# Kernel optimization log

Hardware: AMD Instinct MI355X
Metric: run time of the kernel (lower is better)

## Reference

```python
import jax, jax.numpy as jnp
import numpy as np

COMMITMENT_COST = 0.25
NUM_CODES = 4096
EMBED_DIM = 64


def setup_inputs() -> dict:
    key = jax.random.key(0)
    k1, k2 = jax.random.split(key)
    z_e = jax.random.normal(k1, (65536, EMBED_DIM), dtype=jnp.float32)
    embeddings = jax.random.normal(k2, (NUM_CODES, EMBED_DIM), dtype=jnp.float32)
    return {"z_e": z_e, "embeddings": embeddings}


def reference(z_e, embeddings):
    # Squared Euclidean distances; argmin is identical to torch.cdist argmin.
    # d2[n,k] = |z_e[n]|^2 - 2 z_e[n].e[k] + |e[k]|^2
    z_sq = jnp.sum(z_e * z_e, axis=-1, keepdims=True)            # [N,1]
    e_sq = jnp.sum(embeddings * embeddings, axis=-1)              # [K]
    d2 = z_sq - 2.0 * jnp.einsum('nd,kd->nk', z_e, embeddings) + e_sq  # [N,K]
    indices = jnp.argmin(d2, axis=-1)                             # [N] int
    z_q = embeddings[indices]                                     # [N,D] gather

    # commitment loss = mse(stop_grad(z_q), z_e)
    commitment_loss = COMMITMENT_COST * jnp.mean(
        (jax.lax.stop_gradient(z_q) - z_e) ** 2)

    # straight-through estimator
    z_q_st = z_e + jax.lax.stop_gradient(z_q - z_e)

    # code usage stats: one-hot mean == normalized histogram (scatter-add)
    n = z_e.shape[0]
    counts = jnp.zeros((NUM_CODES,), dtype=jnp.float32).at[indices].add(1.0)
    avg_probs = counts / n
    perplexity = jnp.exp(-jnp.sum(avg_probs * jnp.log(avg_probs + 1e-10)))
    n_active = jnp.sum(avg_probs > 0.001)

    return z_q_st, indices, commitment_loss, perplexity, n_active
```

## Files before the change

kernel.cpp:

```cpp
#include <hip/hip_runtime.h>
#include <math.h>

#define D 64
#define K 4096
#define MARGIN 0.015f
#define KSPLIT 4
#define CPH (K / 16 / KSPLIT)

typedef float f32x4 __attribute__((ext_vector_type(4)));
typedef short bf16x8 __attribute__((ext_vector_type(8)));

static __device__ inline unsigned short f2bf(float x) {
  unsigned u = __builtin_bit_cast(unsigned, x);
  unsigned r = (u + 0x7FFF + ((u >> 16) & 1)) >> 16;
  return (unsigned short)r;
}
static __device__ inline float bf2f(unsigned short s) {
  unsigned u = ((unsigned)s) << 16;
  return __builtin_bit_cast(float, u);
}

__global__ __launch_bounds__(256) void esq_kernel(const float* __restrict__ emb,
                                                  float* __restrict__ e_sq) {
  int k = blockIdx.x * 256 + threadIdx.x;
  if (k >= K) return;
  const float* e = emb + (size_t)k * D;
  float s = 0.f;
#pragma unroll
  for (int d = 0; d < D; ++d) s = fmaf(e[d], e[d], s);
  e_sq[k] = s;
}

__global__ __launch_bounds__(256) void esplit_kernel(const float* __restrict__ emb,
                                                     short* __restrict__ e_hi,
                                                     short* __restrict__ e_lo) {
  int i = blockIdx.x * 256 + threadIdx.x;
  if (i >= (K / 16) * 2 * 64) return;
  int lane = i & 63;
  int t = (i >> 6) & 1;
  int c = i >> 7;
  int quad = lane >> 4, col = lane & 15;
  const float* src = emb + (size_t)(c * 16 + col) * D + t * 32 + quad * 8;
  f32x4 u0 = *(const f32x4*)src;
  f32x4 u1 = *(const f32x4*)(src + 4);
  bf16x8 h, l;
#pragma unroll
  for (int j = 0; j < 8; ++j) {
    float x = (j < 4) ? u0[j] : u1[j - 4];
    unsigned short hb = f2bf(x);
    h[j] = (short)hb;
    l[j] = (short)f2bf(x - bf2f(hb));
  }
  size_t dst = ((size_t)i) * 8;
  *(bf16x8*)(e_hi + dst) = h;
  *(bf16x8*)(e_lo + dst) = l;
}

__global__ __launch_bounds__(256, 2) void dist_kernel(const float* __restrict__ z_e,
                                                      const short* __restrict__ e_hi,
                                                      const short* __restrict__ e_lo,
                                                      const float* __restrict__ esq,
                                                      float* __restrict__ pbest,
                                                      float* __restrict__ psec,
                                                      int* __restrict__ pidx) {
  const int tid = threadIdx.x;
  const int wv = tid >> 6;
  const int lane = tid & 63;
  const int quad = lane >> 4, col = lane & 15;
  const int rowbase = blockIdx.x * 128 + wv * 32;
  const int half = blockIdx.y;
  const int c0 = half * CPH;

  bf16x8 a_hi[2][2], a_lo[2][2];
#pragma unroll
  for (int s = 0; s < 2; ++s) {
#pragma unroll
    for (int t = 0; t < 2; ++t) {
      const float* zr = z_e + (size_t)(rowbase + s * 16 + col) * D + t * 32 + quad * 8;
      f32x4 u0 = *(const f32x4*)zr;
      f32x4 u1 = *(const f32x4*)(zr + 4);
#pragma unroll
      for (int j = 0; j < 8; ++j) {
        float x = (j < 4) ? u0[j] : u1[j - 4];
        unsigned short hb = f2bf(x);
        a_hi[s][t][j] = (short)hb;
        a_lo[s][t][j] = (short)f2bf(x - bf2f(hb));
      }
    }
  }

  float best[8], second[8];
  int bidx[8];
#pragma unroll
  for (int i = 0; i < 8; ++i) {
    best[i] = __builtin_inff();
    second[i] = __builtin_inff();
    bidx[i] = 0;
  }

  const size_t lofs = (size_t)lane * 8;

  for (int cc = 0; cc < CPH; ++cc) {
    const int c = c0 + cc;
    const bf16x8 bh0 = *(const bf16x8*)(e_hi + (size_t)(c * 2 + 0) * 512 + lofs);
    const bf16x8 bh1 = *(const bf16x8*)(e_hi + (size_t)(c * 2 + 1) * 512 + lofs);
    const bf16x8 bl0 = *(const bf16x8*)(e_lo + (size_t)(c * 2 + 0) * 512 + lofs);
    const bf16x8 bl1 = *(const bf16x8*)(e_lo + (size_t)(c * 2 + 1) * 512 + lofs);
    const float esql = esq[c * 16 + col];
    const int code = c * 16 + col;

    f32x4 acc0 = {0.f, 0.f, 0.f, 0.f};
    f32x4 acc1 = {0.f, 0.f, 0.f, 0.f};
    acc0 = __builtin_amdgcn_mfma_f32_16x16x32_bf16(a_hi[0][0], bh0, acc0, 0, 0, 0);
    acc1 = __builtin_amdgcn_mfma_f32_16x16x32_bf16(a_hi[1][0], bh0, acc1, 0, 0, 0);
    acc0 = __builtin_amdgcn_mfma_f32_16x16x32_bf16(a_lo[0][0], bh0, acc0, 0, 0, 0);
    acc1 = __builtin_amdgcn_mfma_f32_16x16x32_bf16(a_lo[1][0], bh0, acc1, 0, 0, 0);
    acc0 = __builtin_amdgcn_mfma_f32_16x16x32_bf16(a_hi[0][0], bl0, acc0, 0, 0, 0);
    acc1 = __builtin_amdgcn_mfma_f32_16x16x32_bf16(a_hi[1][0], bl0, acc1, 0, 0, 0);
    acc0 = __builtin_amdgcn_mfma_f32_16x16x32_bf16(a_hi[0][1], bh1, acc0, 0, 0, 0);
    acc1 = __builtin_amdgcn_mfma_f32_16x16x32_bf16(a_hi[1][1], bh1, acc1, 0, 0, 0);
    acc0 = __builtin_amdgcn_mfma_f32_16x16x32_bf16(a_lo[0][1], bh1, acc0, 0, 0, 0);
    acc1 = __builtin_amdgcn_mfma_f32_16x16x32_bf16(a_lo[1][1], bh1, acc1, 0, 0, 0);
    acc0 = __builtin_amdgcn_mfma_f32_16x16x32_bf16(a_hi[0][1], bl1, acc0, 0, 0, 0);
    acc1 = __builtin_amdgcn_mfma_f32_16x16x32_bf16(a_hi[1][1], bl1, acc1, 0, 0, 0);

#pragma unroll
    for (int r = 0; r < 4; ++r) {
      float q = fmaf(-2.f, acc0[r], esql);
      float ob = best[r];
      best[r] = fminf(ob, q);
      second[r] = __builtin_amdgcn_fmed3f(ob, q, second[r]);
      bidx[r] = (q < ob) ? code : bidx[r];
    }
#pragma unroll
    for (int r = 0; r < 4; ++r) {
      float q = fmaf(-2.f, acc1[r], esql);
      float ob = best[4 + r];
      best[4 + r] = fminf(ob, q);
      second[4 + r] = __builtin_amdgcn_fmed3f(ob, q, second[4 + r]);
      bidx[4 + r] = (q < ob) ? code : bidx[4 + r];
    }
  }

#pragma unroll
  for (int i = 0; i < 8; ++i) {
    float b = best[i], s2 = second[i];
    int ix = bidx[i];
#pragma unroll
    for (int off = 1; off < 16; off <<= 1) {
      float ob = __shfl_xor(b, off);
      float os = __shfl_xor(s2, off);
      int oi = __shfl_xor(ix, off);
      float ns = fminf(fminf(s2, os), fmaxf(b, ob));
      if (ob < b || (ob == b && oi < ix)) ix = oi;
      b = fminf(b, ob);
      s2 = ns;
    }
    if (col == 0) {
      int row = rowbase + (i >> 2) * 16 + quad * 4 + (i & 3);
      size_t o = (size_t)half * 65536 + row;
      pbest[o] = b;
      psec[o] = s2;
      pidx[o] = ix;
    }
  }
}

__global__ __launch_bounds__(256) void merge_kernel(const float* __restrict__ pbest,
                                                    const float* __restrict__ psec,
                                                    const int* __restrict__ pidx,
                                                    int* __restrict__ best_idx,
                                                    int* __restrict__ worklist,
                                                    int* __restrict__ nwork,
                                                    int N) {
  int row = blockIdx.x * 256 + threadIdx.x;
  float b = pbest[row];
  float s2 = psec[row];
  int ix = pidx[row];
#pragma unroll
  for (int h = 1; h < KSPLIT; ++h) {
    size_t o = (size_t)h * 65536 + row;
    float bh = pbest[o];
    float sh = psec[o];
    int ih = pidx[o];
    s2 = fminf(fminf(s2, sh), fmaxf(b, bh));
    if (bh < b) ix = ih;
    b = fminf(b, bh);
  }
  best_idx[row] = ix;
  if (s2 - b < MARGIN) {
    int slot = atomicAdd(nwork, 1);
    worklist[slot] = row;
  }
}

__global__ __launch_bounds__(256, 1) void resolve_kernel(const float* __restrict__ z_e,
                                                         const float* __restrict__ emb,
                                                         const float* __restrict__ esq,
                                                         const float* __restrict__ pbest,
                                                         const float* __restrict__ psec,
                                                         const int* __restrict__ pidx,
                                                         const int* __restrict__ worklist,
                                                         const int* __restrict__ nwork,
                                                         int* __restrict__ best_idx) {
  const int tid = threadIdx.x;
  const int wave = tid >> 6;
  const int lane = tid & 63;
  const int wgid = blockIdx.x * 4 + wave;

  __shared__ float zs[4][D];
  const int n = *nwork;

  for (int j = wgid; j < n; j += 1024) {
    const int row = worklist[j];
    if (lane < 16) ((f32x4*)zs[wave])[lane] = *((const f32x4*)(z_e + (size_t)row * D) + lane);

    float pb[KSPLIT], ps[KSPLIT];
    int pi[KSPLIT];
    float B = __builtin_inff();
#pragma unroll
    for (int h = 0; h < KSPLIT; ++h) {
      size_t o = (size_t)h * 65536 + row;
      pb[h] = pbest[o];
      ps[h] = psec[o];
      pi[h] = pidx[o];
      B = fminf(B, pb[h]);
    }
    const float lim = B + MARGIN;

    float bv = __builtin_inff();
    int bi = 0;
#pragma unroll
    for (int h = 0; h < KSPLIT; ++h) {
      if (ps[h] < lim) {
        float hb = __builtin_inff();
        int hx = 0;
        for (int t = 0; t < 16; ++t) {
          int c = h * 1024 + t * 64 + lane;
          const f32x4* er = (const f32x4*)(emb + (size_t)c * D);
          f32x4 a = {0.f, 0.f, 0.f, 0.f};
#pragma unroll
          for (int i = 0; i < 16; ++i)
            a = __builtin_elementwise_fma(er[i], ((const f32x4*)zs[wave])[i], a);
          float dot = (a[0] + a[1]) + (a[2] + a[3]);
          float q = fmaf(-2.f, dot, esq[c]);
          if (q < hb) { hb = q; hx = c; }
        }
#pragma unroll
        for (int off = 32; off > 0; off >>= 1) {
          float ov = __shfl_down(hb, off);
          int oi = __shfl_down(hx, off);
          if (ov < hb || (ov == hb && oi < hx)) { hb = ov; hx = oi; }
        }
        hb = __shfl(hb, 0);
        hx = __shfl(hx, 0);
        if (hb < bv || (hb == bv && hx < bi)) { bv = hb; bi = hx; }
      } else if (pb[h] < lim) {
        int c = pi[h];
        float p = emb[(size_t)c * D + lane] * zs[wave][lane];
#pragma unroll
        for (int off = 1; off < 64; off <<= 1) p += __shfl_xor(p, off);
        float q = fmaf(-2.f, p, esq[c]);
        if (q < bv || (q == bv && c < bi)) { bv = q; bi = c; }
      }
    }
    if (lane == 0) best_idx[row] = bi;
  }
}

__global__ __launch_bounds__(256) void finalize_kernel(const float* __restrict__ z_e,
                                                       const float* __restrict__ emb,
                                                       const int* __restrict__ best_idx,
                                                       float* __restrict__ out_zq,
                                                       float* __restrict__ out_idx,
                                                       int* __restrict__ counts,
                                                       float* __restrict__ block_loss) {
  const int tid = threadIdx.x;
  const int wave = tid >> 6;
  const int lane = tid & 63;
  const int row = blockIdx.x * 4 + wave;

  int bidx = best_idx[row];
  float ze = z_e[(size_t)row * D + lane];
  float zq = emb[(size_t)bidx * D + lane];
  float st = ze + (zq - ze);
  out_zq[(size_t)row * D + lane] = st;

  float diff = zq - ze;
  float sq = diff * diff;
#pragma unroll
  for (int off = 32; off > 0; off >>= 1) sq += __shfl_down(sq, off);

  __shared__ float ls[4];
  if (lane == 0) {
    ls[wave] = sq;
    out_idx[row] = (float)bidx;
    atomicAdd(&counts[bidx], 1);
  }
  __syncthreads();
  if (tid == 0) block_loss[blockIdx.x] = ls[0] + ls[1] + ls[2] + ls[3];
}

__global__ __launch_bounds__(1024) void stats_kernel(const float* __restrict__ block_loss,
                                                     int nblocks,
                                                     const int* __restrict__ counts,
                                                     float* __restrict__ out_scalars,
                                                     int N) {
  const int tid = threadIdx.x;
  const int wave = tid >> 6;
  const int lane = tid & 63;

  float lsum = 0.f;
  for (int i = tid; i < nblocks; i += 1024) lsum += block_loss[i];

  float ent = 0.f;
  int act = 0;
  const float invN = 1.0f / (float)N;
  for (int k = tid; k < K; k += 1024) {
    float p = (float)counts[k] * invN;
    ent += p * logf(p + 1e-10f);
    act += (p > 0.001f) ? 1 : 0;
  }

#pragma unroll
  for (int off = 32; off > 0; off >>= 1) {
    lsum += __shfl_down(lsum, off);
    ent += __shfl_down(ent, off);
    act += __shfl_down(act, off);
  }

  __shared__ float sl[16], se[16];
  __shared__ int sa[16];
  if (lane == 0) { sl[wave] = lsum; se[wave] = ent; sa[wave] = act; }
  __syncthreads();
  if (tid == 0) {
    float L = 0.f, E = 0.f;
    int A = 0;
#pragma unroll
    for (int w = 0; w < 16; ++w) { L += sl[w]; E += se[w]; A += sa[w]; }
    out_scalars[0] = 0.25f * L / ((float)N * (float)D);
    out_scalars[1] = expf(-E);
    out_scalars[2] = (float)A;
  }
}

extern "C" void kernel_launch(void* const* d_in, const int* in_sizes, int n_in,
                              void* d_out, int out_size, void* d_ws, size_t ws_size,
                              hipStream_t stream) {
  const float* z_e = (const float*)d_in[0];
  const float* emb = (const float*)d_in[1];
  const int N = in_sizes[0] / D;

  float* out = (float*)d_out;
  float* out_zq = out;
  float* out_idx = out + (size_t)N * D;
  float* out_scalars = out + (size_t)N * (D + 1);

  char* ws = (char*)d_ws;
  size_t o = 0;
  int* counts = (int*)(ws + o);      o += 16384;
  int* nwork = (int*)(ws + o);       o += 256;
  float* esq = (float*)(ws + o);     o += 16384;
  short* e_hi = (short*)(ws + o);    o += (size_t)K * D * 2;
  short* e_lo = (short*)(ws + o);    o += (size_t)K * D * 2;
  float* pbest = (float*)(ws + o);   o += (size_t)KSPLIT * N * 4;
  float* psec = (float*)(ws + o);    o += (size_t)KSPLIT * N * 4;
  int* pidx = (int*)(ws + o);        o += (size_t)KSPLIT * N * 4;
  int* best_idx = (int*)(ws + o);    o += (size_t)N * 4;
  int* worklist = (int*)(ws + o);    o += (size_t)N * 4;
  float* block_loss = (float*)(ws + o);

  hipMemsetAsync(counts, 0, 16384 + 256, stream);

  esq_kernel<<<K / 256, 256, 0, stream>>>(emb, esq);
  esplit_kernel<<<(K / 16) * 2 * 64 / 256, 256, 0, stream>>>(emb, e_hi, e_lo);
  dist_kernel<<<dim3(N / 128, KSPLIT), 256, 0, stream>>>(z_e, e_hi, e_lo, esq,
                                                         pbest, psec, pidx);
  merge_kernel<<<N / 256, 256, 0, stream>>>(pbest, psec, pidx, best_idx,
                                            worklist, nwork, N);
  resolve_kernel<<<256, 256, 0, stream>>>(z_e, emb, esq, pbest, psec, pidx,
                                          worklist, nwork, best_idx);
  finalize_kernel<<<N / 4, 256, 0, stream>>>(z_e, emb, best_idx, out_zq, out_idx,
                                             counts, block_loss);
  stats_kernel<<<1, 1024, 0, stream>>>(block_loss, N / 4, counts, out_scalars, N);
}
```

Measured before the change: 248.3 us.

## Fold code norm into MFMA accumulator init and fuse merge/resolve/finalize kernels

The dist kernel now seeds the MFMA accumulators with -0.5*|e|^2 and tracks a running max of the dot-minus-half-norm score. This removes the per-element fma from the inner argmin loop, and the scores are rescaled by -2 only at the end. The merge, resolve and finalize kernels are fused into one per-row tail kernel that merges the split partials through wave shuffles. It resolves ambiguous rows in place and writes the outputs, which removes the worklist, the atomic counter and two launches. The trade-off is divergent resolve work inside the finalize grid instead of a compact worklist pass.

```diff
diff --git a/kernel.cpp b/kernel.cpp
--- a/kernel.cpp
+++ b/kernel.cpp
@@ -45,11 +45,18 @@
   f32x4 u1 = *(const f32x4*)(src + 4);
   bf16x8 h, l;
 #pragma unroll
-  for (int j = 0; j < 8; ++j) {
-    float x = (j < 4) ? u0[j] : u1[j - 4];
+  for (int j = 0; j < 4; ++j) {
+    float x = u0[j];
     unsigned short hb = f2bf(x);
     h[j] = (short)hb;
     l[j] = (short)f2bf(x - bf2f(hb));
+  }
+#pragma unroll
+  for (int j = 0; j < 4; ++j) {
+    float x = u1[j];
+    unsigned short hb = f2bf(x);
+    h[4 + j] = (short)hb;
+    l[4 + j] = (short)f2bf(x - bf2f(hb));
   }
   size_t dst = ((size_t)i) * 8;
   *(bf16x8*)(e_hi + dst) = h;
@@ -93,8 +100,8 @@
   int bidx[8];
 #pragma unroll
   for (int i = 0; i < 8; ++i) {
-    best[i] = __builtin_inff();
-    second[i] = __builtin_inff();
+    best[i] = -__builtin_inff();
+    second[i] = -__builtin_inff();
     bidx[i] = 0;
   }
 
@@ -108,9 +115,10 @@
     const bf16x8 bl1 = *(const bf16x8*)(e_lo + (size_t)(c * 2 + 1) * 512 + lofs);
     const float esql = esq[c * 16 + col];
     const int code = c * 16 + col;
-
-    f32x4 acc0 = {0.f, 0.f, 0.f, 0.f};
-    f32x4 acc1 = {0.f, 0.f, 0.f, 0.f};
+    const float ci = -0.5f * esql;
+
+    f32x4 acc0 = {ci, ci, ci, ci};
+    f32x4 acc1 = {ci, ci, ci, ci};
     acc0 = __builtin_amdgcn_mfma_f32_16x16x32_bf16(a_hi[0][0], bh0, acc0, 0, 0, 0);
     acc1 = __builtin_amdgcn_mfma_f32_16x16x32_bf16(a_hi[1][0], bh0, acc1, 0, 0, 0);
     acc0 = __builtin_amdgcn_mfma_f32_16x16x32_bf16(a_lo[0][0], bh0, acc0, 0, 0, 0);
@@ -126,20 +134,27 @@
 
 #pragma unroll
     for (int r = 0; r < 4; ++r) {
-      float q = fmaf(-2.f, acc0[r], esql);
+      float a = acc0[r];
       float ob = best[r];
-      best[r] = fminf(ob, q);
-      second[r] = __builtin_amdgcn_fmed3f(ob, q, second[r]);
-      bidx[r] = (q < ob) ? code : bidx[r];
+      best[r] = fmaxf(ob, a);
+      second[r] = __builtin_amdgcn_fmed3f(ob, a, second[r]);
+      bidx[r] = (a > ob) ? code : bidx[r];
     }
 #pragma unroll
     for (int r = 0; r < 4; ++r) {
-      float q = fmaf(-2.f, acc1[r], esql);
+      float a = acc1[r];
       float ob = best[4 + r];
-      best[4 + r] = fminf(ob, q);
-      second[4 + r] = __builtin_amdgcn_fmed3f(ob, q, second[4 + r]);
-      bidx[4 + r] = (q < ob) ? code : bidx[4 + r];
-    }
+      best[4 + r] = fmaxf(ob, a);
+      second[4 + r] = __builtin_amdgcn_fmed3f(ob, a, second[4 + r]);
+      bidx[4 + r] = (a > ob) ? code : bidx[4 + r];
+    }
+    asm volatile(""
+                 : "+v"(best[0]), "+v"(best[1]), "+v"(best[2]), "+v"(best[3]),
+                   "+v"(best[4]), "+v"(best[5]), "+v"(best[6]), "+v"(best[7]),
+                   "+v"(second[0]), "+v"(second[1]), "+v"(second[2]), "+v"(second[3]),
+                   "+v"(second[4]), "+v"(second[5]), "+v"(second[6]), "+v"(second[7]),
+                   "+v"(bidx[0]), "+v"(bidx[1]), "+v"(bidx[2]), "+v"(bidx[3]),
+                   "+v"(bidx[4]), "+v"(bidx[5]), "+v"(bidx[6]), "+v"(bidx[7]));
   }
 
 #pragma unroll
@@ -151,85 +166,67 @@
       float ob = __shfl_xor(b, off);
       float os = __shfl_xor(s2, off);
       int oi = __shfl_xor(ix, off);
-      float ns = fminf(fminf(s2, os), fmaxf(b, ob));
-      if (ob < b || (ob == b && oi < ix)) ix = oi;
-      b = fminf(b, ob);
+      float ns = fmaxf(fmaxf(s2, os), fminf(b, ob));
+      if (ob > b || (ob == b && oi < ix)) ix = oi;
+      b = fmaxf(b, ob);
       s2 = ns;
     }
     if (col == 0) {
       int row = rowbase + (i >> 2) * 16 + quad * 4 + (i & 3);
       size_t o = (size_t)half * 65536 + row;
-      pbest[o] = b;
-      psec[o] = s2;
+      pbest[o] = -2.f * b;
+      psec[o] = -2.f * s2;
       pidx[o] = ix;
     }
   }
 }
 
-__global__ __launch_bounds__(256) void merge_kernel(const float* __restrict__ pbest,
-                                                    const float* __restrict__ psec,
-                                                    const int* __restrict__ pidx,
-                                                    int* __restrict__ best_idx,
-                                                    int* __restrict__ worklist,
-                                                    int* __restrict__ nwork,
-                                                    int N) {
-  int row = blockIdx.x * 256 + threadIdx.x;
-  float b = pbest[row];
-  float s2 = psec[row];
-  int ix = pidx[row];
-#pragma unroll
-  for (int h = 1; h < KSPLIT; ++h) {
-    size_t o = (size_t)h * 65536 + row;
-    float bh = pbest[o];
-    float sh = psec[o];
-    int ih = pidx[o];
-    s2 = fminf(fminf(s2, sh), fmaxf(b, bh));
-    if (bh < b) ix = ih;
-    b = fminf(b, bh);
-  }
-  best_idx[row] = ix;
-  if (s2 - b < MARGIN) {
-    int slot = atomicAdd(nwork, 1);
-    worklist[slot] = row;
-  }
-}
-
-__global__ __launch_bounds__(256, 1) void resolve_kernel(const float* __restrict__ z_e,
-                                                         const float* __restrict__ emb,
-                                                         const float* __restrict__ esq,
-                                                         const float* __restrict__ pbest,
-                                                         const float* __restrict__ psec,
-                                                         const int* __restrict__ pidx,
-                                                         const int* __restrict__ worklist,
-                                                         const int* __restrict__ nwork,
-                                                         int* __restrict__ best_idx) {
+__global__ __launch_bounds__(256) void tail_kernel(const float* __restrict__ z_e,
+                                                   const float* __restrict__ emb,
+                                                   const float* __restrict__ esq,
+                                                   const float* __restrict__ pbest,
+                                                   const float* __restrict__ psec,
+                                                   const int* __restrict__ pidx,
+                                                   float* __restrict__ out_zq,
+                                                   float* __restrict__ out_idx,
+                                                   int* __restrict__ counts,
+                                                   float* __restrict__ block_loss) {
   const int tid = threadIdx.x;
   const int wave = tid >> 6;
   const int lane = tid & 63;
-  const int wgid = blockIdx.x * 4 + wave;
+  const int row = blockIdx.x * 4 + wave;
 
   __shared__ float zs[4][D];
-  const int n = *nwork;
-
-  for (int j = wgid; j < n; j += 1024) {
-    const int row = worklist[j];
+
+  const int hh = lane & 3;
+  size_t po = (size_t)hh * 65536 + row;
+  float pbl = pbest[po];
+  float psl = psec[po];
+  int pil = pidx[po];
+
+  float pb[KSPLIT], ps[KSPLIT];
+  int pi[KSPLIT];
+#pragma unroll
+  for (int h = 0; h < KSPLIT; ++h) {
+    pb[h] = __shfl(pbl, h);
+    ps[h] = __shfl(psl, h);
+    pi[h] = __shfl(pil, h);
+  }
+
+  float b = pb[0], s2 = ps[0];
+  int bi = pi[0];
+#pragma unroll
+  for (int h = 1; h < KSPLIT; ++h) {
+    s2 = fminf(fminf(s2, ps[h]), fmaxf(b, pb[h]));
+    if (pb[h] < b) bi = pi[h];
+    b = fminf(b, pb[h]);
+  }
+
+  if (s2 - b < MARGIN) {
     if (lane < 16) ((f32x4*)zs[wave])[lane] = *((const f32x4*)(z_e + (size_t)row * D) + lane);
-
-    float pb[KSPLIT], ps[KSPLIT];
-    int pi[KSPLIT];
-    float B = __builtin_inff();
-#pragma unroll
-    for (int h = 0; h < KSPLIT; ++h) {
-      size_t o = (size_t)h * 65536 + row;
-      pb[h] = pbest[o];
-      ps[h] = psec[o];
-      pi[h] = pidx[o];
-      B = fminf(B, pb[h]);
-    }
-    const float lim = B + MARGIN;
-
+    const float lim = b + MARGIN;
     float bv = __builtin_inff();
-    int bi = 0;
+    bi = 0;
 #pragma unroll
     for (int h = 0; h < KSPLIT; ++h) {
       if (ps[h] < lim) {
@@ -264,25 +261,10 @@
         if (q < bv || (q == bv && c < bi)) { bv = q; bi = c; }
       }
     }
-    if (lane == 0) best_idx[row] = bi;
-  }
-}
-
-__global__ __launch_bounds__(256) void finalize_kernel(const float* __restrict__ z_e,
-                                                       const float* __restrict__ emb,
-                                                       const int* __restrict__ best_idx,
-                                                       float* __restrict__ out_zq,
-                                                       float* __restrict__ out_idx,
-                                                       int* __restrict__ counts,
-                                                       float* __restrict__ block_loss) {
-  const int tid = threadIdx.x;
-  const int wave = tid >> 6;
-  const int lane = tid & 63;
-  const int row = blockIdx.x * 4 + wave;
-
-  int bidx = best_idx[row];
+  }
+
   float ze = z_e[(size_t)row * D + lane];
-  float zq = emb[(size_t)bidx * D + lane];
+  float zq = emb[(size_t)bi * D + lane];
   float st = ze + (zq - ze);
   out_zq[(size_t)row * D + lane] = st;
 
@@ -294,8 +276,8 @@
   __shared__ float ls[4];
   if (lane == 0) {
     ls[wave] = sq;
-    out_idx[row] = (float)bidx;
-    atomicAdd(&counts[bidx], 1);
+    out_idx[row] = (float)bi;
+    atomicAdd(&counts[bi], 1);
   }
   __syncthreads();
   if (tid == 0) block_loss[blockIdx.x] = ls[0] + ls[1] + ls[2] + ls[3];
@@ -359,28 +341,21 @@
   char* ws = (char*)d_ws;
   size_t o = 0;
   int* counts = (int*)(ws + o);      o += 16384;
-  int* nwork = (int*)(ws + o);       o += 256;
   float* esq = (float*)(ws + o);     o += 16384;
   short* e_hi = (short*)(ws + o);    o += (size_t)K * D * 2;
   short* e_lo = (short*)(ws + o);    o += (size_t)K * D * 2;
   float* pbest = (float*)(ws + o);   o += (size_t)KSPLIT * N * 4;
   float* psec = (float*)(ws + o);    o += (size_t)KSPLIT * N * 4;
   int* pidx = (int*)(ws + o);        o += (size_t)KSPLIT * N * 4;
-  int* best_idx = (int*)(ws + o);    o += (size_t)N * 4;
-  int* worklist = (int*)(ws + o);    o += (size_t)N * 4;
   float* block_loss = (float*)(ws + o);
 
-  hipMemsetAsync(counts, 0, 16384 + 256, stream);
+  hipMemsetAsync(counts, 0, 16384, stream);
 
   esq_kernel<<<K / 256, 256, 0, stream>>>(emb, esq);
   esplit_kernel<<<(K / 16) * 2 * 64 / 256, 256, 0, stream>>>(emb, e_hi, e_lo);
   dist_kernel<<<dim3(N / 128, KSPLIT), 256, 0, stream>>>(z_e, e_hi, e_lo, esq,
                                                          pbest, psec, pidx);
-  merge_kernel<<<N / 256, 256, 0, stream>>>(pbest, psec, pidx, best_idx,
-                                            worklist, nwork, N);
-  resolve_kernel<<<256, 256, 0, stream>>>(z_e, emb, esq, pbest, psec, pidx,
-                                          worklist, nwork, best_idx);
-  finalize_kernel<<<N / 4, 256, 0, stream>>>(z_e, emb, best_idx, out_zq, out_idx,
-                                             counts, block_loss);
+  tail_kernel<<<N / 4, 256, 0, stream>>>(z_e, emb, esq, pbest, psec, pidx,
+                                         out_zq, out_idx, counts, block_loss);
   stats_kernel<<<1, 1024, 0, stream>>>(block_loss, N / 4, counts, out_scalars, N);
 }
```

Result: slower. 257.2 us (+3.6%).
